# Kernel tuning notes

Measured on AMD Instinct MI355X. Metric: run time of the kernel, lower is better.

The kernel has to match this reference:

```python
import jax, jax.numpy as jnp
import numpy as np

DIM = 1024

def setup_inputs() -> dict:
    key = jax.random.key(0)
    ks = jax.random.split(key, 7)
    s = 1.0 / np.sqrt(DIM)  # roughly match nn.Linear init scale
    return {
        "x": jax.random.normal(ks[0], (4, 2048, DIM), dtype=jnp.float32),
        "Wq": jax.random.normal(ks[1], (DIM, DIM), dtype=jnp.float32) * s,
        "bq": jax.random.normal(ks[2], (DIM,), dtype=jnp.float32) * s,
        "Wk": jax.random.normal(ks[3], (DIM, DIM), dtype=jnp.float32) * s,
        "bk": jax.random.normal(ks[4], (DIM,), dtype=jnp.float32) * s,
        "Wv": jax.random.normal(ks[5], (DIM, DIM), dtype=jnp.float32) * s,
        "bv": jax.random.normal(ks[6], (DIM,), dtype=jnp.float32) * s,
    }

def reference(x, Wq, bq, Wk, bk, Wv, bv):
    # torch Linear: y = x @ W.T + b
    C = x.shape[-1]
    scale = C ** (-0.5)
    q = jnp.einsum('bnc,dc->bnd', x, Wq) + bq
    k = jnp.einsum('bnc,dc->bnd', x, Wk) + bk
    v = jnp.einsum('bnc,dc->bnd', x, Wv) + bv
    attn = jnp.einsum('bnd,bmd->bnm', q, k) * scale  # [B,N,N]
    attn = jax.nn.softmax(attn, axis=-1)
    out = jnp.einsum('bnm,bmd->bnd', attn, v)
    return out
```

## Files before the change

### kernel.cpp

```cpp
#include <hip/hip_runtime.h>

#define SEQ  2048
#define DIM  1024
#define NTOK 8192
#define NQKV 3072

typedef __attribute__((ext_vector_type(8))) __bf16 bf16x8;
typedef __attribute__((ext_vector_type(4))) float  f32x4;

__device__ __forceinline__ unsigned short f2bf(float f) {
    unsigned int u = __float_as_uint(f);
    u += 0x7fffu + ((u >> 16) & 1u);
    return (unsigned short)(u >> 16);
}

__device__ __forceinline__ float bfu2f(unsigned int lo16) {
    return __uint_as_float(lo16 << 16);
}

__device__ __forceinline__ void load_lds_128(const unsigned short* g, unsigned short* l) {
    __builtin_amdgcn_global_load_lds(
        (const __attribute__((address_space(1))) void*)g,
        (__attribute__((address_space(3))) void*)l, 16, 0, 0);
}

template <int MODE, int NF>
__global__ __launch_bounds__(512, 2)
void gemm256(const unsigned short* __restrict__ A, const unsigned short* __restrict__ B,
             void* __restrict__ Cv,
             const float* __restrict__ b0, const float* __restrict__ b1,
             const float* __restrict__ b2, unsigned short* __restrict__ vt,
             const float* __restrict__ inv_rs,
             int K, int lda, int ldb, int ldc,
             long sA, long sB, long sC, float alpha)
{
    constexpr int BN  = NF * 64;
    constexpr int AT  = 256 * 32;
    constexpr int BT  = BN * 32;
    constexpr int LPT = 2 + BN / 128;

    __shared__ unsigned short As[4 * AT];
    __shared__ unsigned short Bs[4 * BT];

    const int tid  = threadIdx.x;
    const int wave = tid >> 6;
    const int lane = tid & 63;
    const int l4   = lane & 15;
    const int lh   = lane >> 4;
    const int wm   = wave >> 2;
    const int wn   = wave & 3;

    const int m0 = blockIdx.x * 256;
    const int n0 = blockIdx.y * BN;
    const int z  = blockIdx.z;
    A += (long)z * sA;
    B += (long)z * sB;

    const unsigned short* Ag0 = A + (long)(m0 + (tid >> 2)) * lda + (tid & 3) * 8;
    const unsigned short* Ag1 = Ag0 + (long)128 * lda;
    const unsigned short* Bg0 = B + (long)(n0 + (tid >> 2)) * ldb + (tid & 3) * 8;
    const unsigned short* Bg1 = Bg0 + (long)128 * ldb;
    unsigned short* Al0 = As + tid * 8;
    unsigned short* Bl0 = Bs + tid * 8;

    const int NT = K >> 5;

    auto stageA = [&](int t) {
        const int bo = (t & 3) * AT;
        load_lds_128(Ag0 + (long)t * 32, Al0 + bo);
        load_lds_128(Ag1 + (long)t * 32, Al0 + bo + 4096);
    };
    auto stageB = [&](int t) {
        const int bo = (t & 3) * BT;
        load_lds_128(Bg0 + (long)t * 32, Bl0 + bo);
        if constexpr (NF == 4)
            load_lds_128(Bg1 + (long)t * 32, Bl0 + bo + 4096);
    };

    const int aoff = (wm * 128 + l4) * 32 + lh * 8;
    const int boff = (wn * (BN / 4) + l4) * 32 + lh * 8;

    f32x4 acc[8][NF] = {};

    stageA(0); stageB(0);
    stageA(1); stageB(1);
    stageA(2); stageB(2);
    asm volatile("s_waitcnt vmcnt(%0)" :: "n"(2 * LPT) : "memory");
    __builtin_amdgcn_s_barrier();

    for (int t = 0; t < NT; ++t) {
        const int bi = t & 3;
        const unsigned short* Ab = As + bi * AT + aoff;
        const unsigned short* Bb = Bs + bi * BT + boff;
        bf16x8 b[NF];

        if constexpr (NF == 4) {
            bf16x8 a[4];
#pragma unroll
            for (int nf = 0; nf < 4; ++nf) b[nf] = *(const bf16x8*)(Bb + nf * 512);
#pragma unroll
            for (int mf = 0; mf < 4; ++mf) a[mf] = *(const bf16x8*)(Ab + mf * 512);
            if (t + 3 < NT) stageA(t + 3);
            __builtin_amdgcn_s_barrier();
            asm volatile("s_waitcnt lgkmcnt(0)" ::: "memory");
            __builtin_amdgcn_sched_barrier(0);
            __builtin_amdgcn_s_setprio(1);
#pragma unroll
            for (int mf = 0; mf < 4; ++mf)
#pragma unroll
                for (int nf = 0; nf < 4; ++nf)
                    acc[mf][nf] = __builtin_amdgcn_mfma_f32_16x16x32_bf16(
                        a[mf], b[nf], acc[mf][nf], 0, 0, 0);
            __builtin_amdgcn_s_setprio(0);
            __builtin_amdgcn_s_barrier();
#pragma unroll
            for (int mf = 0; mf < 4; ++mf) a[mf] = *(const bf16x8*)(Ab + (mf + 4) * 512);
            if (t + 3 < NT) stageB(t + 3);
            __builtin_amdgcn_s_barrier();
            asm volatile("s_waitcnt lgkmcnt(0)" ::: "memory");
            __builtin_amdgcn_sched_barrier(0);
            __builtin_amdgcn_s_setprio(1);
#pragma unroll
            for (int mf = 0; mf < 4; ++mf)
#pragma unroll
                for (int nf = 0; nf < 4; ++nf)
                    acc[mf + 4][nf] = __builtin_amdgcn_mfma_f32_16x16x32_bf16(
                        a[mf], b[nf], acc[mf + 4][nf], 0, 0, 0);
            __builtin_amdgcn_s_setprio(0);
            asm volatile("s_waitcnt vmcnt(%0)" :: "n"(2 * LPT) : "memory");
            __builtin_amdgcn_s_barrier();
        } else {
            bf16x8 a8[8];
#pragma unroll
            for (int nf = 0; nf < NF; ++nf) b[nf] = *(const bf16x8*)(Bb + nf * 512);
#pragma unroll
            for (int mf = 0; mf < 8; ++mf) a8[mf] = *(const bf16x8*)(Ab + mf * 512);
            if (t + 3 < NT) { stageA(t + 3); stageB(t + 3); }
            __builtin_amdgcn_s_barrier();
            asm volatile("s_waitcnt lgkmcnt(0)" ::: "memory");
            __builtin_amdgcn_sched_barrier(0);
            __builtin_amdgcn_s_setprio(1);
#pragma unroll
            for (int mf = 0; mf < 8; ++mf)
#pragma unroll
                for (int nf = 0; nf < NF; ++nf)
                    acc[mf][nf] = __builtin_amdgcn_mfma_f32_16x16x32_bf16(
                        a8[mf], b[nf], acc[mf][nf], 0, 0, 0);
            __builtin_amdgcn_s_setprio(0);
            asm volatile("s_waitcnt vmcnt(%0)" :: "n"(2 * LPT) : "memory");
            __builtin_amdgcn_s_barrier();
        }
    }

    const int r0 = m0 + wm * 128 + lh * 4;
    const int c0 = n0 + wn * (BN / 4) + l4;

    if (MODE == 0) {
        if (n0 >= 2048) {
#pragma unroll
            for (int nf = 0; nf < NF; ++nf) {
                const int d = c0 + nf * 16 - 2048;
                const float bias = b2[d];
#pragma unroll
                for (int mf = 0; mf < 8; ++mf) {
                    const int row = r0 + mf * 16;
                    const int bb = row >> 11;
                    const int mm = row & 2047;
                    ushort4 u;
                    u.x = f2bf(acc[mf][nf][0] + bias);
                    u.y = f2bf(acc[mf][nf][1] + bias);
                    u.z = f2bf(acc[mf][nf][2] + bias);
                    u.w = f2bf(acc[mf][nf][3] + bias);
                    *(ushort4*)(vt + ((long)bb * DIM + d) * SEQ + mm) = u;
                }
            }
        } else {
            unsigned short* C16 = (unsigned short*)Cv;
#pragma unroll
            for (int nf = 0; nf < NF; ++nf) {
                const int col = c0 + nf * 16;
                const float bias = (col >= 1024) ? b1[col - 1024] : b0[col];
#pragma unroll
                for (int mf = 0; mf < 8; ++mf)
#pragma unroll
                    for (int r = 0; r < 4; ++r)
                        C16[(long)(r0 + mf * 16 + r) * ldc + col] =
                            f2bf(acc[mf][nf][r] + bias);
            }
        }
    } else if (MODE == 1) {
        float* C = (float*)Cv + (long)z * sC;
        const float* ir = inv_rs + (long)z * SEQ;
#pragma unroll
        for (int mf = 0; mf < 8; ++mf) {
            const int row = r0 + mf * 16;
            const float4 inv4 = *(const float4*)(ir + row);
#pragma unroll
            for (int nf = 0; nf < NF; ++nf) {
                const int col = c0 + nf * 16;
                C[(long)(row + 0) * ldc + col] = acc[mf][nf][0] * inv4.x;
                C[(long)(row + 1) * ldc + col] = acc[mf][nf][1] * inv4.y;
                C[(long)(row + 2) * ldc + col] = acc[mf][nf][2] * inv4.z;
                C[(long)(row + 3) * ldc + col] = acc[mf][nf][3] * inv4.w;
            }
        }
    } else {
        unsigned short* C16 = (unsigned short*)Cv + (long)z * sC;
#pragma unroll
        for (int nf = 0; nf < NF; ++nf) {
            const int col = c0 + nf * 16;
#pragma unroll
            for (int mf = 0; mf < 8; ++mf)
#pragma unroll
                for (int r = 0; r < 4; ++r)
                    C16[(long)(r0 + mf * 16 + r) * ldc + col] =
                        f2bf(__expf(acc[mf][nf][r] * alpha));
        }
    }
}

__global__ __launch_bounds__(256)
void cvt_x(const float* __restrict__ src, unsigned short* __restrict__ dst, int n4)
{
    int i = blockIdx.x * 256 + threadIdx.x;
    if (i < n4) {
        float4 f = ((const float4*)src)[i];
        ushort4 u;
        u.x = f2bf(f.x); u.y = f2bf(f.y); u.z = f2bf(f.z); u.w = f2bf(f.w);
        ((ushort4*)dst)[i] = u;
    }
}

__global__ __launch_bounds__(256)
void cvt_w3(const float* __restrict__ Wq, const float* __restrict__ Wk,
            const float* __restrict__ Wv, unsigned short* __restrict__ dst)
{
    const int sel = blockIdx.y;
    const float* src = (sel == 0) ? Wq : ((sel == 1) ? Wk : Wv);
    const int i = blockIdx.x * 256 + threadIdx.x;
    float4 f = ((const float4*)src)[i];
    ushort4 u;
    u.x = f2bf(f.x); u.y = f2bf(f.y); u.z = f2bf(f.z); u.w = f2bf(f.w);
    ((ushort4*)(dst + (long)sel * DIM * DIM))[i] = u;
}

__global__ __launch_bounds__(256)
void rowsum_inv(const unsigned short* __restrict__ P, float* __restrict__ inv_rs)
{
    const int row  = blockIdx.x * 4 + (threadIdx.x >> 6);
    const int lane = threadIdx.x & 63;
    const unsigned short* pr = P + (long)row * SEQ;

    float s = 0.f;
#pragma unroll
    for (int it = 0; it < 4; ++it) {
        uint4 u = *(const uint4*)(pr + (it * 64 + lane) * 8);
        s += bfu2f(u.x & 0xffffu) + __uint_as_float(u.x & 0xffff0000u);
        s += bfu2f(u.y & 0xffffu) + __uint_as_float(u.y & 0xffff0000u);
        s += bfu2f(u.z & 0xffffu) + __uint_as_float(u.z & 0xffff0000u);
        s += bfu2f(u.w & 0xffffu) + __uint_as_float(u.w & 0xffff0000u);
    }
    for (int off = 32; off > 0; off >>= 1)
        s += __shfl_xor(s, off);
    if (lane == 0) inv_rs[row] = 1.0f / s;
}

extern "C" void kernel_launch(void* const* d_in, const int* in_sizes, int n_in,
                              void* d_out, int out_size, void* d_ws, size_t ws_size,
                              hipStream_t stream)
{
    const float* x  = (const float*)d_in[0];
    const float* Wq = (const float*)d_in[1];
    const float* bq = (const float*)d_in[2];
    const float* Wk = (const float*)d_in[3];
    const float* bk = (const float*)d_in[4];
    const float* Wv = (const float*)d_in[5];
    const float* bv = (const float*)d_in[6];
    float* out = (float*)d_out;

    char* ws = (char*)d_ws;
    unsigned short* xb   = (unsigned short*)ws;
    unsigned short* Wb   = (unsigned short*)(ws + 16u * 1024 * 1024);
    unsigned short* qkv  = (unsigned short*)(ws + 64u * 1024 * 1024);
    unsigned short* vt   = (unsigned short*)(ws + 112u * 1024 * 1024);
    unsigned short* P    = (unsigned short*)(ws + 128u * 1024 * 1024);
    float*          irs  = (float*)(ws + 160u * 1024 * 1024);

    const float scale = 0.03125f;
    dim3 blk(256);
    dim3 blk512(512);

    cvt_x<<<NTOK * DIM / 4 / 256, blk, 0, stream>>>(x, xb, NTOK * DIM / 4);
    cvt_w3<<<dim3(DIM * DIM / 4 / 256, 3), blk, 0, stream>>>(Wq, Wk, Wv, Wb);

    gemm256<0, 2><<<dim3(NTOK / 256, NQKV / 128), blk512, 0, stream>>>(
        xb, Wb, qkv, bq, bk, bv, vt, nullptr,
        DIM, DIM, DIM, NQKV, 0, 0, 0, 1.0f);

    gemm256<2, 4><<<dim3(SEQ / 256, SEQ / 256, 4), blk512, 0, stream>>>(
        qkv, qkv + 1024, P, nullptr, nullptr, nullptr, nullptr, nullptr,
        DIM, NQKV, NQKV, SEQ,
        (long)SEQ * NQKV, (long)SEQ * NQKV, (long)SEQ * SEQ, scale);

    rowsum_inv<<<NTOK / 4, blk, 0, stream>>>(P, irs);

    gemm256<1, 2><<<dim3(SEQ / 256, DIM / 128, 4), blk512, 0, stream>>>(
        P, vt, out, nullptr, nullptr, nullptr, nullptr, irs,
        SEQ, SEQ, SEQ, DIM,
        (long)SEQ * SEQ, (long)DIM * SEQ, (long)SEQ * DIM, 1.0f);
}
```

Measured before the change: 274.2 us.

## Restructure GEMM to 256x128x64 tiles with XOR-swizzled LDS and triple buffering

Replaces the templated GEMM, which used K-step 32, four LDS buffers and a 4x2 or 4x4 wave grid, with a single 256x128 tile using K-step 64, triple-buffered LDS and a 4x2 wave layout where each wave computes 64x64. An XOR swizzle on the LDS column index is meant to cut bank conflicts on the wider 64-element rows. Each iteration now runs two MFMA half-steps with staged async loads between them, halving the number of loop iterations and barriers per unit of K. The QK^T GEMM now uses BN=128 instead of 256, which doubles its grid size and lowers per-block register pressure but also reduces operand reuse.

```diff
diff --git a/kernel.cpp b/kernel.cpp
--- a/kernel.cpp
+++ b/kernel.cpp
@@ -24,7 +24,11 @@
         (__attribute__((address_space(3))) void*)l, 16, 0, 0);
 }
 
-template <int MODE, int NF>
+#define BAR()    asm volatile("s_barrier" ::: "memory")
+#define WAITL0() do { asm volatile("s_waitcnt lgkmcnt(0)" ::: "memory"); \
+                      __builtin_amdgcn_sched_barrier(0); } while (0)
+
+template <int MODE>
 __global__ __launch_bounds__(512, 2)
 void gemm256(const unsigned short* __restrict__ A, const unsigned short* __restrict__ B,
              void* __restrict__ Cv,
@@ -34,136 +38,119 @@
              int K, int lda, int ldb, int ldc,
              long sA, long sB, long sC, float alpha)
 {
-    constexpr int BN  = NF * 64;
-    constexpr int AT  = 256 * 32;
-    constexpr int BT  = BN * 32;
-    constexpr int LPT = 2 + BN / 128;
-
-    __shared__ unsigned short As[4 * AT];
-    __shared__ unsigned short Bs[4 * BT];
+    constexpr int AT = 256 * 64;
+    constexpr int BT = 128 * 64;
+    __shared__ __align__(16) unsigned short As[3 * AT];
+    __shared__ __align__(16) unsigned short Bs[3 * BT];
 
     const int tid  = threadIdx.x;
     const int wave = tid >> 6;
     const int lane = tid & 63;
     const int l4   = lane & 15;
     const int lh   = lane >> 4;
-    const int wm   = wave >> 2;
-    const int wn   = wave & 3;
+    const int wm   = wave >> 1;
+    const int wn   = wave & 1;
 
     const int m0 = blockIdx.x * 256;
-    const int n0 = blockIdx.y * BN;
+    const int n0 = blockIdx.y * 128;
     const int z  = blockIdx.z;
     A += (long)z * sA;
     B += (long)z * sB;
 
-    const unsigned short* Ag0 = A + (long)(m0 + (tid >> 2)) * lda + (tid & 3) * 8;
-    const unsigned short* Ag1 = Ag0 + (long)128 * lda;
-    const unsigned short* Bg0 = B + (long)(n0 + (tid >> 2)) * ldb + (tid & 3) * 8;
-    const unsigned short* Bg1 = Bg0 + (long)128 * ldb;
-    unsigned short* Al0 = As + tid * 8;
-    unsigned short* Bl0 = Bs + tid * 8;
-
-    const int NT = K >> 5;
-
-    auto stageA = [&](int t) {
-        const int bo = (t & 3) * AT;
-        load_lds_128(Ag0 + (long)t * 32, Al0 + bo);
-        load_lds_128(Ag1 + (long)t * 32, Al0 + bo + 4096);
+    const int r0 = tid >> 3;
+    const int gc = (tid & 7) ^ (r0 & 7);
+    const unsigned short* Ag = A + (long)(m0 + r0) * lda + gc * 8;
+    const unsigned short* Bg = B + (long)(n0 + r0) * ldb + gc * 8;
+    unsigned short* Al = As + tid * 8;
+    unsigned short* Bl = Bs + tid * 8;
+
+    const int NT = K >> 6;
+
+    auto stage = [&](int t, int slot, int ph) {
+        const long kof = (long)t * 64;
+        unsigned short* al = Al + slot * AT;
+        unsigned short* bl = Bl + slot * BT;
+        if (ph == 0) {
+            load_lds_128(Ag + kof,                          al);
+            load_lds_128(Ag + kof + (long)64 * lda,         al + 4096);
+            load_lds_128(Bg + kof,                          bl);
+        } else {
+            load_lds_128(Ag + kof + (long)128 * lda,        al + 8192);
+            load_lds_128(Ag + kof + (long)192 * lda,        al + 12288);
+            load_lds_128(Bg + kof + (long)64 * ldb,         bl + 4096);
+        }
     };
-    auto stageB = [&](int t) {
-        const int bo = (t & 3) * BT;
-        load_lds_128(Bg0 + (long)t * 32, Bl0 + bo);
-        if constexpr (NF == 4)
-            load_lds_128(Bg1 + (long)t * 32, Bl0 + bo + 4096);
-    };
-
-    const int aoff = (wm * 128 + l4) * 32 + lh * 8;
-    const int boff = (wn * (BN / 4) + l4) * 32 + lh * 8;
-
-    f32x4 acc[8][NF] = {};
-
-    stageA(0); stageB(0);
-    stageA(1); stageB(1);
-    stageA(2); stageB(2);
-    asm volatile("s_waitcnt vmcnt(%0)" :: "n"(2 * LPT) : "memory");
-    __builtin_amdgcn_s_barrier();
-
+
+    const int aoff = (wm * 64 + l4) * 64;
+    const int boff = (wn * 64 + l4) * 64;
+    const int cs0  = ((0 + lh) ^ (lane & 7)) * 8;
+    const int cs1  = ((4 + lh) ^ (lane & 7)) * 8;
+
+    f32x4 acc[4][4] = {};
+
+    stage(0, 0, 0); stage(0, 0, 1);
+    stage(1, 1, 0); stage(1, 1, 1);
+    asm volatile("s_waitcnt vmcnt(6)" ::: "memory");
+    BAR();
+
+    int sl = 0;
     for (int t = 0; t < NT; ++t) {
-        const int bi = t & 3;
-        const unsigned short* Ab = As + bi * AT + aoff;
-        const unsigned short* Bb = Bs + bi * BT + boff;
-        bf16x8 b[NF];
-
-        if constexpr (NF == 4) {
-            bf16x8 a[4];
-#pragma unroll
-            for (int nf = 0; nf < 4; ++nf) b[nf] = *(const bf16x8*)(Bb + nf * 512);
-#pragma unroll
-            for (int mf = 0; mf < 4; ++mf) a[mf] = *(const bf16x8*)(Ab + mf * 512);
-            if (t + 3 < NT) stageA(t + 3);
-            __builtin_amdgcn_s_barrier();
-            asm volatile("s_waitcnt lgkmcnt(0)" ::: "memory");
-            __builtin_amdgcn_sched_barrier(0);
-            __builtin_amdgcn_s_setprio(1);
-#pragma unroll
-            for (int mf = 0; mf < 4; ++mf)
-#pragma unroll
-                for (int nf = 0; nf < 4; ++nf)
-                    acc[mf][nf] = __builtin_amdgcn_mfma_f32_16x16x32_bf16(
-                        a[mf], b[nf], acc[mf][nf], 0, 0, 0);
-            __builtin_amdgcn_s_setprio(0);
-            __builtin_amdgcn_s_barrier();
-#pragma unroll
-            for (int mf = 0; mf < 4; ++mf) a[mf] = *(const bf16x8*)(Ab + (mf + 4) * 512);
-            if (t + 3 < NT) stageB(t + 3);
-            __builtin_amdgcn_s_barrier();
-            asm volatile("s_waitcnt lgkmcnt(0)" ::: "memory");
-            __builtin_amdgcn_sched_barrier(0);
-            __builtin_amdgcn_s_setprio(1);
-#pragma unroll
-            for (int mf = 0; mf < 4; ++mf)
-#pragma unroll
-                for (int nf = 0; nf < 4; ++nf)
-                    acc[mf + 4][nf] = __builtin_amdgcn_mfma_f32_16x16x32_bf16(
-                        a[mf], b[nf], acc[mf + 4][nf], 0, 0, 0);
-            __builtin_amdgcn_s_setprio(0);
-            asm volatile("s_waitcnt vmcnt(%0)" :: "n"(2 * LPT) : "memory");
-            __builtin_amdgcn_s_barrier();
-        } else {
-            bf16x8 a8[8];
-#pragma unroll
-            for (int nf = 0; nf < NF; ++nf) b[nf] = *(const bf16x8*)(Bb + nf * 512);
-#pragma unroll
-            for (int mf = 0; mf < 8; ++mf) a8[mf] = *(const bf16x8*)(Ab + mf * 512);
-            if (t + 3 < NT) { stageA(t + 3); stageB(t + 3); }
-            __builtin_amdgcn_s_barrier();
-            asm volatile("s_waitcnt lgkmcnt(0)" ::: "memory");
-            __builtin_amdgcn_sched_barrier(0);
-            __builtin_amdgcn_s_setprio(1);
-#pragma unroll
-            for (int mf = 0; mf < 8; ++mf)
-#pragma unroll
-                for (int nf = 0; nf < NF; ++nf)
-                    acc[mf][nf] = __builtin_amdgcn_mfma_f32_16x16x32_bf16(
-                        a8[mf], b[nf], acc[mf][nf], 0, 0, 0);
-            __builtin_amdgcn_s_setprio(0);
-            asm volatile("s_waitcnt vmcnt(%0)" :: "n"(2 * LPT) : "memory");
-            __builtin_amdgcn_s_barrier();
-        }
-    }
-
-    const int r0 = m0 + wm * 128 + lh * 4;
-    const int c0 = n0 + wn * (BN / 4) + l4;
+        const unsigned short* Ab = As + sl * AT + aoff;
+        const unsigned short* Bb = Bs + sl * BT + boff;
+        const int st = (sl >= 1) ? sl - 1 : 2;
+        const bool pf = (t + 2 < NT);
+        bf16x8 a[4], b[4];
+
+#pragma unroll
+        for (int mf = 0; mf < 4; ++mf) a[mf] = *(const bf16x8*)(Ab + mf * 1024 + cs0);
+#pragma unroll
+        for (int nf = 0; nf < 4; ++nf) b[nf] = *(const bf16x8*)(Bb + nf * 1024 + cs0);
+        if (pf) stage(t + 2, st, 0);
+        BAR();
+        WAITL0();
+        __builtin_amdgcn_s_setprio(1);
+#pragma unroll
+        for (int mf = 0; mf < 4; ++mf)
+#pragma unroll
+            for (int nf = 0; nf < 4; ++nf)
+                acc[mf][nf] = __builtin_amdgcn_mfma_f32_16x16x32_bf16(
+                    a[mf], b[nf], acc[mf][nf], 0, 0, 0);
+        __builtin_amdgcn_s_setprio(0);
+
+#pragma unroll
+        for (int mf = 0; mf < 4; ++mf) a[mf] = *(const bf16x8*)(Ab + mf * 1024 + cs1);
+#pragma unroll
+        for (int nf = 0; nf < 4; ++nf) b[nf] = *(const bf16x8*)(Bb + nf * 1024 + cs1);
+        if (pf) stage(t + 2, st, 1);
+        BAR();
+        WAITL0();
+        __builtin_amdgcn_s_setprio(1);
+#pragma unroll
+        for (int mf = 0; mf < 4; ++mf)
+#pragma unroll
+            for (int nf = 0; nf < 4; ++nf)
+                acc[mf][nf] = __builtin_amdgcn_mfma_f32_16x16x32_bf16(
+                    a[mf], b[nf], acc[mf][nf], 0, 0, 0);
+        __builtin_amdgcn_s_setprio(0);
+
+        if (t < NT - 2) asm volatile("s_waitcnt vmcnt(6)" ::: "memory");
+        else            asm volatile("s_waitcnt vmcnt(0)" ::: "memory");
+        BAR();
+        sl = (sl == 2) ? 0 : sl + 1;
+    }
+
+    const int r0c = m0 + wm * 64 + lh * 4;
+    const int c0c = n0 + wn * 64 + l4;
 
     if (MODE == 0) {
         if (n0 >= 2048) {
 #pragma unroll
-            for (int nf = 0; nf < NF; ++nf) {
-                const int d = c0 + nf * 16 - 2048;
+            for (int nf = 0; nf < 4; ++nf) {
+                const int d = c0c + nf * 16 - 2048;
                 const float bias = b2[d];
 #pragma unroll
-                for (int mf = 0; mf < 8; ++mf) {
-                    const int row = r0 + mf * 16;
+                for (int mf = 0; mf < 4; ++mf) {
+                    const int row = r0c + mf * 16;
                     const int bb = row >> 11;
                     const int mm = row & 2047;
                     ushort4 u;
@@ -177,14 +164,14 @@
         } else {
             unsigned short* C16 = (unsigned short*)Cv;
 #pragma unroll
-            for (int nf = 0; nf < NF; ++nf) {
-                const int col = c0 + nf * 16;
+            for (int nf = 0; nf < 4; ++nf) {
+                const int col = c0c + nf * 16;
                 const float bias = (col >= 1024) ? b1[col - 1024] : b0[col];
 #pragma unroll
-                for (int mf = 0; mf < 8; ++mf)
+                for (int mf = 0; mf < 4; ++mf)
 #pragma unroll
                     for (int r = 0; r < 4; ++r)
-                        C16[(long)(r0 + mf * 16 + r) * ldc + col] =
+                        C16[(long)(r0c + mf * 16 + r) * ldc + col] =
                             f2bf(acc[mf][nf][r] + bias);
             }
         }
@@ -192,12 +179,12 @@
         float* C = (float*)Cv + (long)z * sC;
         const float* ir = inv_rs + (long)z * SEQ;
 #pragma unroll
-        for (int mf = 0; mf < 8; ++mf) {
-            const int row = r0 + mf * 16;
+        for (int mf = 0; mf < 4; ++mf) {
+            const int row = r0c + mf * 16;
             const float4 inv4 = *(const float4*)(ir + row);
 #pragma unroll
-            for (int nf = 0; nf < NF; ++nf) {
-                const int col = c0 + nf * 16;
+            for (int nf = 0; nf < 4; ++nf) {
+                const int col = c0c + nf * 16;
                 C[(long)(row + 0) * ldc + col] = acc[mf][nf][0] * inv4.x;
                 C[(long)(row + 1) * ldc + col] = acc[mf][nf][1] * inv4.y;
                 C[(long)(row + 2) * ldc + col] = acc[mf][nf][2] * inv4.z;
@@ -207,13 +194,13 @@
     } else {
         unsigned short* C16 = (unsigned short*)Cv + (long)z * sC;
 #pragma unroll
-        for (int nf = 0; nf < NF; ++nf) {
-            const int col = c0 + nf * 16;
-#pragma unroll
-            for (int mf = 0; mf < 8; ++mf)
+        for (int nf = 0; nf < 4; ++nf) {
+            const int col = c0c + nf * 16;
+#pragma unroll
+            for (int mf = 0; mf < 4; ++mf)
 #pragma unroll
                 for (int r = 0; r < 4; ++r)
-                    C16[(long)(r0 + mf * 16 + r) * ldc + col] =
+                    C16[(long)(r0c + mf * 16 + r) * ldc + col] =
                         f2bf(__expf(acc[mf][nf][r] * alpha));
         }
     }
@@ -293,18 +280,18 @@
     cvt_x<<<NTOK * DIM / 4 / 256, blk, 0, stream>>>(x, xb, NTOK * DIM / 4);
     cvt_w3<<<dim3(DIM * DIM / 4 / 256, 3), blk, 0, stream>>>(Wq, Wk, Wv, Wb);
 
-    gemm256<0, 2><<<dim3(NTOK / 256, NQKV / 128), blk512, 0, stream>>>(
+    gemm256<0><<<dim3(NTOK / 256, NQKV / 128), blk512, 0, stream>>>(
         xb, Wb, qkv, bq, bk, bv, vt, nullptr,
         DIM, DIM, DIM, NQKV, 0, 0, 0, 1.0f);
 
-    gemm256<2, 4><<<dim3(SEQ / 256, SEQ / 256, 4), blk512, 0, stream>>>(
+    gemm256<2><<<dim3(SEQ / 256, SEQ / 128, 4), blk512, 0, stream>>>(
         qkv, qkv + 1024, P, nullptr, nullptr, nullptr, nullptr, nullptr,
         DIM, NQKV, NQKV, SEQ,
         (long)SEQ * NQKV, (long)SEQ * NQKV, (long)SEQ * SEQ, scale);
 
     rowsum_inv<<<NTOK / 4, blk, 0, stream>>>(P, irs);
 
-    gemm256<1, 2><<<dim3(SEQ / 256, DIM / 128, 4), blk512, 0, stream>>>(
+    gemm256<1><<<dim3(SEQ / 256, DIM / 128, 4), blk512, 0, stream>>>(
         P, vt, out, nullptr, nullptr, nullptr, nullptr, irs,
         SEQ, SEQ, SEQ, DIM,
         (long)SEQ * SEQ, (long)DIM * SEQ, (long)SEQ * DIM, 1.0f);
```

After: 255.9 us. 6.7% less time.
